# Kernel tuning notes

Measured on AMD Instinct MI355X. Metric: run time of the kernel, lower is better.

Reference implementation:

```python
import jax, jax.numpy as jnp
import numpy as np

B, S, H = 1, 2048, 1024   # batch, seq_len, hidden_size
E, K, I = 8, 2, 1024      # num_experts, top_k, intermediate_size


def setup_inputs() -> dict:
    key = jax.random.key(0)
    ks = jax.random.split(key, 5)
    x = jax.random.normal(ks[0], (B, S, H), dtype=jnp.float32)
    gate_w = jax.random.normal(ks[1], (H, E), dtype=jnp.float32) * 0.02
    wg = jax.random.normal(ks[2], (E, H, I), dtype=jnp.float32) * 0.02  # gate_proj per expert
    wu = jax.random.normal(ks[3], (E, H, I), dtype=jnp.float32) * 0.02  # up_proj per expert
    wd = jax.random.normal(ks[4], (E, I, H), dtype=jnp.float32) * 0.02  # down_proj per expert
    return {"x": x, "gate_w": gate_w, "wg": wg, "wu": wu, "wd": wd}


def _moe(x, gate_w, wg, wu, wd):
    b, s, h = x.shape
    n = b * s
    logits = jnp.einsum('bsh,he->bse', x, gate_w)          # [B,S,E]
    top_vals, sel = jax.lax.top_k(logits, K)               # [B,S,K]
    rweights = jax.nn.softmax(top_vals, axis=-1)           # [B,S,K]
    x_flat = x.reshape(n, h)
    sel_flat = sel.reshape(n, K)
    rw_flat = rweights.reshape(n, K)

    def expert_body(out, params):
        e, Wg, Wu, Wd = params
        hit = jnp.any(sel_flat == e, axis=-1)              # [N] tokens routed to e in any slot
        # stable argsort: hit tokens first, in ascending original index order
        perm = jnp.argsort(jnp.logical_not(hit))
        tokens = x_flat[perm]                              # [N,H] (row j = j-th token of token_indices)
        y = jnp.einsum('ni,ih->nh', jax.nn.silu(tokens @ Wg) * (tokens @ Wu), Wd)  # [N,H]
        contrib = jnp.zeros_like(out)
        for k in range(K):
            km = sel_flat[:, k] == e                       # [N]
            # original does output_flat[k_indices] += w * expert_output[:len(k_indices)]
            # i.e. j-th token of k_indices gets expert_output row j
            ranks = jnp.clip(jnp.cumsum(km) - 1, 0, n - 1)
            w = jnp.where(km, rw_flat[:, k], 0.0)
            contrib = contrib + w[:, None] * y[ranks]
        return out + contrib, None

    out, _ = jax.lax.scan(expert_body, jnp.zeros_like(x_flat),
                          (jnp.arange(E), wg, wu, wd))
    output = out.reshape(b, s, h)

    # aux metrics (match LoadBalancedRouter)
    probs = jax.nn.softmax(logits, axis=-1)
    usage = probs.mean(axis=(0, 1))                        # [E]
    balance_loss = jnp.var(usage, ddof=1) * E              # torch.var is unbiased
    su = jnp.sort(usage)
    idx = jnp.arange(1, E + 1, dtype=usage.dtype)
    gini = 2.0 * (idx * su).sum() / (E * su.sum()) - (E + 1.0) / E
    entropy = -(probs * jnp.log(probs + 1e-10)).sum(-1).mean()
    return output, balance_loss, gini, entropy


def reference(x, gate_w, wg, wu, wd):
    return _moe(x, gate_w, wg, wu, wd)
```

## Files before the change

kernel.cpp:

```cpp
#include <hip/hip_runtime.h>
#include <stdint.h>

#define TOKENS 2048
#define HID 1024
#define NE 8

typedef __attribute__((ext_vector_type(8))) short bf16x8;
typedef __attribute__((ext_vector_type(4))) float f32x4;

__device__ __forceinline__ unsigned short f2bf(float f) {
  unsigned int u = __float_as_uint(f);
  return (unsigned short)((u + 0x7fffu + ((u >> 16) & 1u)) >> 16);
}

__device__ __forceinline__ void gload16(const void* g, void* l) {
  __builtin_amdgcn_global_load_lds((const __attribute__((address_space(1))) void*)g,
                                   (__attribute__((address_space(3))) void*)l, 16, 0, 0);
}

__global__ __launch_bounds__(256) void k_pre(
    const float* __restrict__ x, const float* __restrict__ gw,
    const float* __restrict__ wg, const float* __restrict__ wu, const float* __restrict__ wd,
    unsigned short* __restrict__ wgt, unsigned short* __restrict__ wut,
    unsigned short* __restrict__ wdt,
    int* __restrict__ sel, float* __restrict__ rw,
    float* __restrict__ probs, float* __restrict__ ent) {
  __shared__ float tile[64][65];
  const int bid = blockIdx.x;
  const int tid = threadIdx.x;

  if (bid < 6144) {
    const int bx = bid & 15;
    const int by = (bid >> 4) & 15;
    const int e = (bid >> 8) & 7;
    const int tensor = bid >> 11;
    const float* src = (tensor == 0 ? wg : tensor == 1 ? wu : wd) + ((size_t)e << 20);
    unsigned short* dst = (tensor == 0 ? wgt : tensor == 1 ? wut : wdt) + ((size_t)e << 20);
    const int tr = tid >> 4, tc = (tid & 15) * 4;
#pragma unroll
    for (int p = 0; p < 4; ++p) {
      const int row = p * 16 + tr;
      const float4 v = *(const float4*)(src + (size_t)(by * 64 + row) * 1024 + bx * 64 + tc);
      tile[row][tc] = v.x; tile[row][tc + 1] = v.y; tile[row][tc + 2] = v.z; tile[row][tc + 3] = v.w;
    }
    __syncthreads();
#pragma unroll
    for (int p = 0; p < 4; ++p) {
      const int row = p * 16 + tr;
      const ushort4 o = make_ushort4(f2bf(tile[tc + 0][row]), f2bf(tile[tc + 1][row]),
                                     f2bf(tile[tc + 2][row]), f2bf(tile[tc + 3][row]));
      *(ushort4*)(dst + (size_t)(bx * 64 + row) * 1024 + by * 64 + tc) = o;
    }
    return;
  }

  const int w = tid >> 6;
  const int lane = tid & 63;
  const int t = (bid - 6144) * 4 + w;

  const float4* x4 = (const float4*)(x + (size_t)t * HID);
  const float4* gw4 = (const float4*)gw;

  float acc[NE];
#pragma unroll
  for (int e = 0; e < NE; ++e) acc[e] = 0.f;

#pragma unroll
  for (int i = 0; i < 4; ++i) {
    const int idx4 = i * 64 + lane;
    const float4 xv = x4[idx4];
    float4 g[8];
#pragma unroll
    for (int k = 0; k < 8; ++k) g[k] = gw4[(size_t)idx4 * 8 + k];
    const float xs[4] = {xv.x, xv.y, xv.z, xv.w};
#pragma unroll
    for (int c = 0; c < 4; ++c) {
      acc[0] += xs[c] * g[c * 2].x;
      acc[1] += xs[c] * g[c * 2].y;
      acc[2] += xs[c] * g[c * 2].z;
      acc[3] += xs[c] * g[c * 2].w;
      acc[4] += xs[c] * g[c * 2 + 1].x;
      acc[5] += xs[c] * g[c * 2 + 1].y;
      acc[6] += xs[c] * g[c * 2 + 1].z;
      acc[7] += xs[c] * g[c * 2 + 1].w;
    }
  }

#pragma unroll
  for (int e = 0; e < NE; ++e) {
#pragma unroll
    for (int msk = 32; msk >= 1; msk >>= 1) acc[e] += __shfl_xor(acc[e], msk, 64);
  }

  float mx = acc[0];
#pragma unroll
  for (int e = 1; e < NE; ++e) mx = fmaxf(mx, acc[e]);

  const int e8 = lane & 7;
  float my = acc[0];
#pragma unroll
  for (int k = 1; k < NE; ++k) if (e8 == k) my = acc[k];
  const float exl = expf(my - mx);
  float S = exl;
#pragma unroll
  for (int msk = 1; msk <= 4; msk <<= 1) S += __shfl_xor(S, msk, 64);
  const float pp = exl / S;
  if (lane < 8) probs[t * NE + lane] = pp;
  float ev = -pp * logf(pp + 1e-10f);
#pragma unroll
  for (int msk = 1; msk <= 4; msk <<= 1) ev += __shfl_xor(ev, msk, 64);

  if (lane == 0) {
    ent[t] = ev;
    int b0 = 0; float v0 = acc[0];
#pragma unroll
    for (int e = 1; e < NE; ++e) if (acc[e] > v0) { v0 = acc[e]; b0 = e; }
    int b1 = -1; float v1 = 0.f;
#pragma unroll
    for (int e = 0; e < NE; ++e) {
      if (e != b0 && (b1 < 0 || acc[e] > v1)) { v1 = acc[e]; b1 = e; }
    }
    const float w1e = expf(v1 - v0);
    const float s2 = 1.f + w1e;
    sel[t * 2] = b0; sel[t * 2 + 1] = b1;
    rw[t * 2] = 1.f / s2; rw[t * 2 + 1] = w1e / s2;
  }
}

__global__ void k_aux(const int* __restrict__ sel, int* __restrict__ cnt,
                      int* __restrict__ hit_list, int* __restrict__ rowidx,
                      const float* __restrict__ probs, const float* __restrict__ ent,
                      float* __restrict__ dout) {
  const int tid = threadIdx.x;

  if (blockIdx.x == 8) {
    __shared__ float red[256][NE];
    __shared__ float rede[256];
    const float4* p4 = (const float4*)probs;
    float pa[NE];
#pragma unroll
    for (int e = 0; e < NE; ++e) pa[e] = 0.f;
    float ea = 0.f;
    for (int t = tid; t < TOKENS; t += 256) {
      const float4 a = p4[t * 2];
      const float4 b = p4[t * 2 + 1];
      pa[0] += a.x; pa[1] += a.y; pa[2] += a.z; pa[3] += a.w;
      pa[4] += b.x; pa[5] += b.y; pa[6] += b.z; pa[7] += b.w;
      ea += ent[t];
    }
#pragma unroll
    for (int e = 0; e < NE; ++e) red[tid][e] = pa[e];
    rede[tid] = ea;
    __syncthreads();
    for (int s = 128; s >= 1; s >>= 1) {
      if (tid < s) {
#pragma unroll
        for (int e = 0; e < NE; ++e) red[tid][e] += red[tid + s][e];
        rede[tid] += rede[tid + s];
      }
      __syncthreads();
    }
    if (tid == 0) {
      float us[NE];
      for (int e = 0; e < NE; ++e) us[e] = red[0][e] / (float)TOKENS;
      float mean = 0.f;
      for (int e = 0; e < NE; ++e) mean += us[e];
      mean /= (float)NE;
      float var = 0.f;
      for (int e = 0; e < NE; ++e) { const float d = us[e] - mean; var += d * d; }
      var /= (float)(NE - 1);
      const float bl = var * (float)NE;
      for (int i = 1; i < NE; ++i) {
        const float key = us[i]; int j = i - 1;
        while (j >= 0 && us[j] > key) { us[j + 1] = us[j]; --j; }
        us[j + 1] = key;
      }
      float num = 0.f, den = 0.f;
      for (int i = 0; i < NE; ++i) { num += (float)(i + 1) * us[i]; den += us[i]; }
      const float gini = 2.f * num / ((float)NE * den) - (float)(NE + 1) / (float)NE;
      dout[(size_t)TOKENS * HID] = bl;
      dout[(size_t)TOKENS * HID + 1] = gini;
      dout[(size_t)TOKENS * HID + 2] = rede[0] / (float)TOKENS;
    }
    return;
  }

  const int e = blockIdx.x;
  __shared__ unsigned long long ssum[256];
  __shared__ unsigned long long csumA[256];
  __shared__ unsigned long long csumB[256];

  int s0[8], s1[8];
  unsigned long long mine = 0ull;
  unsigned long long cA = 0ull, cB = 0ull;
#pragma unroll
  for (int j = 0; j < 8; ++j) {
    const int t = tid * 8 + j;
    s0[j] = sel[2 * t]; s1[j] = sel[2 * t + 1];
#pragma unroll
    for (int q = 0; q < 4; ++q) {
      cA += ((unsigned long long)((s0[j] == q) + (s1[j] == q))) << (16 * q);
      cB += ((unsigned long long)((s0[j] == q + 4) + (s1[j] == q + 4))) << (16 * q);
    }
    const unsigned long long k0 = (s0[j] == e) ? 1ull : 0ull;
    const unsigned long long k1 = (s1[j] == e) ? 1ull : 0ull;
    mine += (k0 | k1) | (k0 << 21) | (k1 << 42);
  }
  ssum[tid] = mine;
  csumA[tid] = cA;
  csumB[tid] = cB;
  __syncthreads();
  for (int s = 128; s >= 1; s >>= 1) {
    if (tid < s) { csumA[tid] += csumA[tid + s]; csumB[tid] += csumB[tid + s]; }
    __syncthreads();
  }
  const unsigned long long totA = csumA[0];
  const unsigned long long totB = csumB[0];
  int tc[NE];
#pragma unroll
  for (int q = 0; q < 4; ++q) {
    tc[q] = (int)((totA >> (16 * q)) & 0xFFFFull);
    tc[q + 4] = (int)((totB >> (16 * q)) & 0xFFFFull);
  }
  if (e == 0 && tid < NE) cnt[tid] = tc[tid];
  int poff = 0;
#pragma unroll
  for (int q = 0; q < NE; ++q) if (q < e) poff += (tc[q] + 127) & ~127;

  for (int s = 1; s < 256; s <<= 1) {
    const unsigned long long v = (tid >= s) ? ssum[tid - s] : 0ull;
    __syncthreads();
    ssum[tid] += v;
    __syncthreads();
  }
  const unsigned long long excl = (tid > 0) ? ssum[tid - 1] : 0ull;
  int hc = (int)(excl & 0x1FFFFFull);
  int c0 = (int)((excl >> 21) & 0x1FFFFFull);
  int c1 = (int)((excl >> 42) & 0x1FFFFFull);
#pragma unroll
  for (int j = 0; j < 8; ++j) {
    const int t = tid * 8 + j;
    const int k0 = (s0[j] == e), k1 = (s1[j] == e);
    if (k0 | k1) { hit_list[poff + hc] = t; ++hc; }
    if (k0) { rowidx[2 * t] = poff + c0; ++c0; }
    if (k1) { rowidx[2 * t + 1] = poff + c1; ++c1; }
  }
}

__global__ void k_gather(const float* __restrict__ x, const int* __restrict__ hit_list,
                         const int* __restrict__ cnt, unsigned short* __restrict__ A) {
  const int mb = blockIdx.x, e = blockIdx.y;
  const int ce = cnt[e];
  const int pc = (ce + 127) & ~127;
  if (mb * 8 >= pc) return;
  int poff = 0;
  for (int q = 0; q < e; ++q) poff += (cnt[q] + 127) & ~127;
  const int tid = threadIdx.x;
#pragma unroll
  for (int i = 0; i < 8; ++i) {
    const int rr = mb * 8 + i;
    unsigned short* dst = A + (size_t)(poff + rr) * 1024 + tid * 4;
    if (rr < ce) {
      const int t = hit_list[poff + rr];
      const float4 v = *(const float4*)(x + (size_t)t * 1024 + tid * 4);
      *(ushort4*)dst = make_ushort4(f2bf(v.x), f2bf(v.y), f2bf(v.z), f2bf(v.w));
    } else {
      *(ushort4*)dst = make_ushort4(0, 0, 0, 0);
    }
  }
}

__global__ __launch_bounds__(256, 4) void k_gemm1(
    const unsigned short* __restrict__ A, const unsigned short* __restrict__ wgt,
    const unsigned short* __restrict__ wut, const int* __restrict__ cnt,
    unsigned short* __restrict__ T) {
  const int nb = blockIdx.x, mb = blockIdx.y, e = blockIdx.z;
  const int ce = cnt[e];
  if (mb * 128 >= ce) return;
  int poff = 0;
  for (int q = 0; q < e; ++q) poff += (cnt[q] + 127) & ~127;

  const unsigned short* Ab = A + (size_t)(poff + mb * 128) * 1024;
  const unsigned short* Bg = wgt + ((size_t)e << 20) + ((size_t)nb << 16);
  const unsigned short* Bu = wut + ((size_t)e << 20) + ((size_t)nb << 16);

  __shared__ __align__(16) short lds[3][8192];

  const int tid = threadIdx.x;
  const int lane = tid & 63;
  const int w = tid >> 6;
  const int wm = w & 1, wn = w >> 1;
  const int r = lane & 15, gq = lane >> 4;
  const int slot = gq ^ ((r >> 1) & 3);
  const int srow = lane >> 2;
  const int skoff = ((lane & 3) ^ ((lane >> 3) & 3)) << 3;

  f32x4 accg[4][2], accu[4][2];
  const f32x4 fz = {0.f, 0.f, 0.f, 0.f};
#pragma unroll
  for (int i = 0; i < 4; ++i)
#pragma unroll
    for (int j = 0; j < 2; ++j) { accg[i][j] = fz; accu[i][j] = fz; }

  auto stage = [&](int kt, int b) {
#pragma unroll
    for (int q = 0; q < 4; ++q) {
      const int gseg = w + q * 4;
      const unsigned short* sb;
      int seg;
      if (gseg < 8) { sb = Ab; seg = gseg; }
      else if (gseg < 12) { sb = Bg; seg = gseg - 8; }
      else { sb = Bu; seg = gseg - 12; }
      gload16(sb + (size_t)(seg * 16 + srow) * 1024 + kt * 32 + skoff,
              &lds[b][gseg * 512]);
    }
  };

  stage(0, 0); stage(1, 1); stage(2, 2);
  int curb = 0;
  for (int kt = 0; kt < 32; ++kt) {
    if (kt < 30)      { asm volatile("s_waitcnt vmcnt(8)" ::: "memory"); }
    else if (kt == 30){ asm volatile("s_waitcnt vmcnt(4)" ::: "memory"); }
    else              { asm volatile("s_waitcnt vmcnt(0)" ::: "memory"); }
    __builtin_amdgcn_sched_barrier(0);
    __builtin_amdgcn_s_barrier();
    __builtin_amdgcn_sched_barrier(0);

    const short* La = &lds[curb][0];
    const short* Lg = &lds[curb][4096];
    const short* Lu = &lds[curb][6144];
    bf16x8 af[4], gf[2], uf[2];
#pragma unroll
    for (int f = 0; f < 4; ++f)
      af[f] = *(const bf16x8*)(La + (wm * 64 + f * 16 + r) * 32 + slot * 8);
#pragma unroll
    for (int f = 0; f < 2; ++f) {
      gf[f] = *(const bf16x8*)(Lg + (wn * 32 + f * 16 + r) * 32 + slot * 8);
      uf[f] = *(const bf16x8*)(Lu + (wn * 32 + f * 16 + r) * 32 + slot * 8);
    }
    asm volatile("s_waitcnt lgkmcnt(0)" ::: "memory");
    __builtin_amdgcn_sched_barrier(0);
    __builtin_amdgcn_s_barrier();
    __builtin_amdgcn_sched_barrier(0);
    if (kt <= 28) stage(kt + 3, curb);

#pragma unroll
    for (int i = 0; i < 4; ++i)
#pragma unroll
      for (int j = 0; j < 2; ++j) {
        accg[i][j] = __builtin_amdgcn_mfma_f32_16x16x32_bf16(af[i], gf[j], accg[i][j], 0, 0, 0);
        accu[i][j] = __builtin_amdgcn_mfma_f32_16x16x32_bf16(af[i], uf[j], accu[i][j], 0, 0, 0);
      }
    curb = (curb == 2) ? 0 : curb + 1;
  }

  const size_t rowbase = (size_t)(poff + mb * 128);
#pragma unroll
  for (int i = 0; i < 4; ++i)
#pragma unroll
    for (int j = 0; j < 2; ++j) {
      const int col = nb * 64 + wn * 32 + j * 16 + r;
#pragma unroll
      for (int rr = 0; rr < 4; ++rr) {
        const int rowt = wm * 64 + i * 16 + gq * 4 + rr;
        const float gv = accg[i][j][rr];
        const float uv = accu[i][j][rr];
        const float sv = gv / (1.f + expf(-gv)) * uv;
        T[(rowbase + rowt) * 1024 + col] = f2bf(sv);
      }
    }
}

__global__ __launch_bounds__(256, 4) void k_gemm2(
    const unsigned short* __restrict__ T, const unsigned short* __restrict__ wdt,
    const int* __restrict__ cnt, float* __restrict__ Y) {
  const int nb = blockIdx.x, mb = blockIdx.y, e = blockIdx.z;
  const int ce = cnt[e];
  if (mb * 128 >= ce) return;
  int poff = 0;
  for (int q = 0; q < e; ++q) poff += (cnt[q] + 127) & ~127;

  const unsigned short* Ab = T + (size_t)(poff + mb * 128) * 1024;
  const unsigned short* Bd = wdt + ((size_t)e << 20) + ((size_t)nb << 16);

  __shared__ __align__(16) short lds[3][6144];

  const int tid = threadIdx.x;
  const int lane = tid & 63;
  const int w = tid >> 6;
  const int wm = w & 1, wn = w >> 1;
  const int r = lane & 15, gq = lane >> 4;
  const int slot = gq ^ ((r >> 1) & 3);
  const int srow = lane >> 2;
  const int skoff = ((lane & 3) ^ ((lane >> 3) & 3)) << 3;

  f32x4 acc[4][2];
  const f32x4 fz = {0.f, 0.f, 0.f, 0.f};
#pragma unroll
  for (int i = 0; i < 4; ++i)
#pragma unroll
    for (int j = 0; j < 2; ++j) acc[i][j] = fz;

  auto stage = [&](int kt, int b) {
#pragma unroll
    for (int q = 0; q < 3; ++q) {
      const int gseg = w + q * 4;
      const unsigned short* sb;
      int seg;
      if (gseg < 8) { sb = Ab; seg = gseg; }
      else { sb = Bd; seg = gseg - 8; }
      gload16(sb + (size_t)(seg * 16 + srow) * 1024 + kt * 32 + skoff,
              &lds[b][gseg * 512]);
    }
  };

  stage(0, 0); stage(1, 1); stage(2, 2);
  int curb = 0;
  for (int kt = 0; kt < 32; ++kt) {
    if (kt < 30)      { asm volatile("s_waitcnt vmcnt(6)" ::: "memory"); }
    else if (kt == 30){ asm volatile("s_waitcnt vmcnt(3)" ::: "memory"); }
    else              { asm volatile("s_waitcnt vmcnt(0)" ::: "memory"); }
    __builtin_amdgcn_sched_barrier(0);
    __builtin_amdgcn_s_barrier();
    __builtin_amdgcn_sched_barrier(0);

    const short* La = &lds[curb][0];
    const short* Lb = &lds[curb][4096];
    bf16x8 af[4], bfr[2];
#pragma unroll
    for (int f = 0; f < 4; ++f)
      af[f] = *(const bf16x8*)(La + (wm * 64 + f * 16 + r) * 32 + slot * 8);
#pragma unroll
    for (int f = 0; f < 2; ++f)
      bfr[f] = *(const bf16x8*)(Lb + (wn * 32 + f * 16 + r) * 32 + slot * 8);
    asm volatile("s_waitcnt lgkmcnt(0)" ::: "memory");
    __builtin_amdgcn_sched_barrier(0);
    __builtin_amdgcn_s_barrier();
    __builtin_amdgcn_sched_barrier(0);
    if (kt <= 28) stage(kt + 3, curb);

#pragma unroll
    for (int i = 0; i < 4; ++i)
#pragma unroll
      for (int j = 0; j < 2; ++j)
        acc[i][j] = __builtin_amdgcn_mfma_f32_16x16x32_bf16(af[i], bfr[j], acc[i][j], 0, 0, 0);
    curb = (curb == 2) ? 0 : curb + 1;
  }

  const size_t rowbase = (size_t)(poff + mb * 128);
#pragma unroll
  for (int i = 0; i < 4; ++i)
#pragma unroll
    for (int j = 0; j < 2; ++j) {
      const int col = nb * 64 + wn * 32 + j * 16 + r;
#pragma unroll
      for (int rr = 0; rr < 4; ++rr) {
        const int rowt = wm * 64 + i * 16 + gq * 4 + rr;
        Y[(rowbase + rowt) * 1024 + col] = acc[i][j][rr];
      }
    }
}

__global__ void k_out(const float* __restrict__ Y, const int* __restrict__ rowidx,
                      const float* __restrict__ rw, float* __restrict__ out) {
  const int t = blockIdx.x;
  const int tid = threadIdx.x;
  const int r0 = rowidx[2 * t], r1 = rowidx[2 * t + 1];
  const float w0 = rw[2 * t], w1 = rw[2 * t + 1];
  const float4 y0 = *(const float4*)(Y + (size_t)r0 * HID + tid * 4);
  const float4 y1 = *(const float4*)(Y + (size_t)r1 * HID + tid * 4);
  float4 o;
  o.x = w0 * y0.x + w1 * y1.x;
  o.y = w0 * y0.y + w1 * y1.y;
  o.z = w0 * y0.z + w1 * y1.z;
  o.w = w0 * y0.w + w1 * y1.w;
  *(float4*)(out + (size_t)t * HID + tid * 4) = o;
}

extern "C" void kernel_launch(void* const* d_in, const int* in_sizes, int n_in,
                              void* d_out, int out_size, void* d_ws, size_t ws_size,
                              hipStream_t stream) {
  const float* x = (const float*)d_in[0];
  const float* gw = (const float*)d_in[1];
  const float* wg = (const float*)d_in[2];
  const float* wu = (const float*)d_in[3];
  const float* wd = (const float*)d_in[4];
  float* out = (float*)d_out;

  char* p = (char*)d_ws;
  unsigned short* wgt = (unsigned short*)p;
  unsigned short* wut = (unsigned short*)(p + 16777216);
  float* Y = (float*)p;
  unsigned short* wdt = (unsigned short*)(p + 33554432);
  unsigned short* A = (unsigned short*)(p + 50331648);
  unsigned short* T = (unsigned short*)(p + 62914560);
  char* q = p + 75497472;
  float* probs = (float*)q; q += 65536;
  float* ent = (float*)q; q += 8192;
  int* sel = (int*)q; q += 16384;
  float* rwp = (float*)q; q += 16384;
  int* rowidx = (int*)q; q += 16384;
  int* hit_list = (int*)q; q += 20480;
  int* cnt = (int*)q;

  k_pre<<<6656, 256, 0, stream>>>(x, gw, wg, wu, wd, wgt, wut, wdt, sel, rwp, probs, ent);
  k_aux<<<9, 256, 0, stream>>>(sel, cnt, hit_list, rowidx, probs, ent, out);
  k_gather<<<dim3(256, 8), 256, 0, stream>>>(x, hit_list, cnt, A);
  k_gemm1<<<dim3(16, 16, 8), 256, 0, stream>>>(A, wgt, wut, cnt, T);
  k_gemm2<<<dim3(16, 16, 8), 256, 0, stream>>>(T, wdt, cnt, Y);
  k_out<<<2048, 256, 0, stream>>>(Y, rowidx, rwp, out);
}
```

Measured before the change: 124.7 us.

## Move down-proj weight conversion into gemm1 launch to overlap with compute

The fp32-to-bf16 transpose of the down-projection weights moves out of the preprocessing kernel into an extra z-slice of the gemm1 grid. There, 256 blocks each convert 8 tiles while the other blocks run the gate/up GEMM. The aim is to hide that conversion traffic behind GEMM compute and to shorten the serial pre-kernel. The risk is that the conversion blocks compete with GEMM blocks for bandwidth and CU slots, and per-block tile loops with syncs may serialize.

```diff
diff --git a/kernel.cpp b/kernel.cpp
--- a/kernel.cpp
+++ b/kernel.cpp
@@ -20,22 +20,21 @@
 
 __global__ __launch_bounds__(256) void k_pre(
     const float* __restrict__ x, const float* __restrict__ gw,
-    const float* __restrict__ wg, const float* __restrict__ wu, const float* __restrict__ wd,
+    const float* __restrict__ wg, const float* __restrict__ wu,
     unsigned short* __restrict__ wgt, unsigned short* __restrict__ wut,
-    unsigned short* __restrict__ wdt,
     int* __restrict__ sel, float* __restrict__ rw,
     float* __restrict__ probs, float* __restrict__ ent) {
   __shared__ float tile[64][65];
   const int bid = blockIdx.x;
   const int tid = threadIdx.x;
 
-  if (bid < 6144) {
+  if (bid < 4096) {
     const int bx = bid & 15;
     const int by = (bid >> 4) & 15;
     const int e = (bid >> 8) & 7;
-    const int tensor = bid >> 11;
-    const float* src = (tensor == 0 ? wg : tensor == 1 ? wu : wd) + ((size_t)e << 20);
-    unsigned short* dst = (tensor == 0 ? wgt : tensor == 1 ? wut : wdt) + ((size_t)e << 20);
+    const int tensor = (bid >> 11) & 1;
+    const float* src = (tensor == 0 ? wg : wu) + ((size_t)e << 20);
+    unsigned short* dst = (tensor == 0 ? wgt : wut) + ((size_t)e << 20);
     const int tr = tid >> 4, tc = (tid & 15) * 4;
 #pragma unroll
     for (int p = 0; p < 4; ++p) {
@@ -56,7 +55,7 @@
 
   const int w = tid >> 6;
   const int lane = tid & 63;
-  const int t = (bid - 6144) * 4 + w;
+  const int t = (bid - 4096) * 4 + w;
 
   const float4* x4 = (const float4*)(x + (size_t)t * HID);
   const float4* gw4 = (const float4*)gw;
@@ -273,7 +272,39 @@
 __global__ __launch_bounds__(256, 4) void k_gemm1(
     const unsigned short* __restrict__ A, const unsigned short* __restrict__ wgt,
     const unsigned short* __restrict__ wut, const int* __restrict__ cnt,
-    unsigned short* __restrict__ T) {
+    unsigned short* __restrict__ T,
+    const float* __restrict__ wd, unsigned short* __restrict__ wdt) {
+  __shared__ __align__(16) short lds[3][8192];
+  const int tid = threadIdx.x;
+
+  if (blockIdx.z == 8) {
+    float (*tile)[65] = (float(*)[65])&lds[0][0];
+    const int cb = blockIdx.y * 16 + blockIdx.x;
+    const int tr = tid >> 4, tc = (tid & 15) * 4;
+    for (int i = 0; i < 8; ++i) {
+      const int ti = cb * 8 + i;
+      const int bx = ti & 15, by = (ti >> 4) & 15, e = ti >> 8;
+      const float* src = wd + ((size_t)e << 20);
+      unsigned short* dst = wdt + ((size_t)e << 20);
+#pragma unroll
+      for (int p = 0; p < 4; ++p) {
+        const int row = p * 16 + tr;
+        const float4 v = *(const float4*)(src + (size_t)(by * 64 + row) * 1024 + bx * 64 + tc);
+        tile[row][tc] = v.x; tile[row][tc + 1] = v.y; tile[row][tc + 2] = v.z; tile[row][tc + 3] = v.w;
+      }
+      __syncthreads();
+#pragma unroll
+      for (int p = 0; p < 4; ++p) {
+        const int row = p * 16 + tr;
+        const ushort4 o = make_ushort4(f2bf(tile[tc + 0][row]), f2bf(tile[tc + 1][row]),
+                                       f2bf(tile[tc + 2][row]), f2bf(tile[tc + 3][row]));
+        *(ushort4*)(dst + (size_t)(bx * 64 + row) * 1024 + by * 64 + tc) = o;
+      }
+      __syncthreads();
+    }
+    return;
+  }
+
   const int nb = blockIdx.x, mb = blockIdx.y, e = blockIdx.z;
   const int ce = cnt[e];
   if (mb * 128 >= ce) return;
@@ -284,9 +315,6 @@
   const unsigned short* Bg = wgt + ((size_t)e << 20) + ((size_t)nb << 16);
   const unsigned short* Bu = wut + ((size_t)e << 20) + ((size_t)nb << 16);
 
-  __shared__ __align__(16) short lds[3][8192];
-
-  const int tid = threadIdx.x;
   const int lane = tid & 63;
   const int w = tid >> 6;
   const int wm = w & 1, wn = w >> 1;
@@ -503,10 +531,10 @@
   int* hit_list = (int*)q; q += 20480;
   int* cnt = (int*)q;
 
-  k_pre<<<6656, 256, 0, stream>>>(x, gw, wg, wu, wd, wgt, wut, wdt, sel, rwp, probs, ent);
+  k_pre<<<4608, 256, 0, stream>>>(x, gw, wg, wu, wgt, wut, sel, rwp, probs, ent);
   k_aux<<<9, 256, 0, stream>>>(sel, cnt, hit_list, rowidx, probs, ent, out);
   k_gather<<<dim3(256, 8), 256, 0, stream>>>(x, hit_list, cnt, A);
-  k_gemm1<<<dim3(16, 16, 8), 256, 0, stream>>>(A, wgt, wut, cnt, T);
+  k_gemm1<<<dim3(16, 16, 9), 256, 0, stream>>>(A, wgt, wut, cnt, T, wd, wdt);
   k_gemm2<<<dim3(16, 16, 8), 256, 0, stream>>>(T, wdt, cnt, Y);
   k_out<<<2048, 256, 0, stream>>>(Y, rowidx, rwp, out);
 }
```

Result: faster. 118.8 us (-4.8%).
